# Kernel tuning notes

Hardware: AMD Instinct MI355X
Metric: run time of the kernel (lower is better)

The kernel has to match this reference:

```python
import jax, jax.numpy as jnp
import numpy as np

N_NODES = 10000
N_EDGES = 80000
N_GRAPHS = 64
HEADS = 8
F_IN = 128
D1, D2, D3 = 512, 256, 128  # per-head (and output, concat=False) widths
OUT_DIM = 10


def _lin(key, fin, fout):
    kw, kb = jax.random.split(key)
    w = jax.random.normal(kw, (fin, fout), dtype=jnp.float32) * 0.05
    b = jax.random.normal(kb, (fout,), dtype=jnp.float32) * 0.05
    return w, b


def setup_inputs() -> dict:
    key = jax.random.key(0)
    ks = jax.random.split(key, 24)
    x = jax.random.normal(ks[0], (N_NODES, F_IN), dtype=jnp.float32)
    edge_index = jax.random.randint(ks[1], (2, N_EDGES), 0, N_NODES, dtype=jnp.int64)
    batch = jnp.sort(jax.random.randint(ks[2], (N_NODES,), 0, N_GRAPHS, dtype=jnp.int64))
    d = {"x": x, "edge_index": edge_index, "batch": batch}
    # conv1: 128 -> heads*512 (q,k,v), skip 128 -> 512
    d["w_q1"], d["b_q1"] = _lin(ks[3], F_IN, HEADS * D1)
    d["w_k1"], d["b_k1"] = _lin(ks[4], F_IN, HEADS * D1)
    d["w_v1"], d["b_v1"] = _lin(ks[5], F_IN, HEADS * D1)
    d["w_s1"], d["b_s1"] = _lin(ks[6], F_IN, D1)
    # conv2: 512 -> heads*256, skip 512 -> 256
    d["w_q2"], d["b_q2"] = _lin(ks[7], D1, HEADS * D2)
    d["w_k2"], d["b_k2"] = _lin(ks[8], D1, HEADS * D2)
    d["w_v2"], d["b_v2"] = _lin(ks[9], D1, HEADS * D2)
    d["w_s2"], d["b_s2"] = _lin(ks[10], D1, D2)
    # conv3: 256 -> heads*128, skip 256 -> 128
    d["w_q3"], d["b_q3"] = _lin(ks[11], D2, HEADS * D3)
    d["w_k3"], d["b_k3"] = _lin(ks[12], D2, HEADS * D3)
    d["w_v3"], d["b_v3"] = _lin(ks[13], D2, HEADS * D3)
    d["w_s3"], d["b_s3"] = _lin(ks[14], D2, D3)
    # global attention gate + final fc
    d["w_g"], d["b_g"] = _lin(ks[15], D3, 1)
    d["w_fc"], d["b_fc"] = _lin(ks[16], D3, OUT_DIM)
    return d


def _seg_softmax(a, seg, n):
    m = jax.ops.segment_max(a, seg, num_segments=n)
    e = jnp.exp(a - m[seg])
    s = jax.ops.segment_sum(e, seg, num_segments=n)
    return e / (s[seg] + 1e-16)


def _tconv(x, edge_index, wq, bq, wk, bk, wv, bv, ws, bs):
    # PyG TransformerConv, concat=False, root_weight=True, no edge features
    n = x.shape[0]
    c = wq.shape[1] // HEADS
    q = (x @ wq + bq).reshape(n, HEADS, c)
    k = (x @ wk + bk).reshape(n, HEADS, c)
    v = (x @ wv + bv).reshape(n, HEADS, c)
    src, dst = edge_index[0], edge_index[1]
    a = jnp.einsum('ehc,ehc->eh', q[dst], k[src]) / jnp.sqrt(jnp.float32(c))
    alpha = _seg_softmax(a, dst, n)                                  # [E, H]
    out = jax.ops.segment_sum(v[src] * alpha[..., None], dst, num_segments=n)
    return out.mean(axis=1) + (x @ ws + bs)                          # mean over heads + skip


def reference(x, edge_index, batch,
              w_q1, b_q1, w_k1, b_k1, w_v1, b_v1, w_s1, b_s1,
              w_q2, b_q2, w_k2, b_k2, w_v2, b_v2, w_s2, b_s2,
              w_q3, b_q3, w_k3, b_k3, w_v3, b_v3, w_s3, b_s3,
              w_g, b_g, w_fc, b_fc):
    h = jax.nn.elu(_tconv(x, edge_index, w_q1, b_q1, w_k1, b_k1, w_v1, b_v1, w_s1, b_s1))
    h = jax.nn.elu(_tconv(h, edge_index, w_q2, b_q2, w_k2, b_k2, w_v2, b_v2, w_s2, b_s2))
    h = jax.nn.elu(_tconv(h, edge_index, w_q3, b_q3, w_k3, b_k3, w_v3, b_v3, w_s3, b_s3))
    # GlobalAttention pooling: softmax(gate) over nodes within each graph
    gate = h @ w_g + b_g                                             # [N, 1]
    gate = _seg_softmax(gate, batch, N_GRAPHS)
    g = jax.ops.segment_sum(gate * h, batch, num_segments=N_GRAPHS)  # [G, D3]
    return g @ w_fc + b_fc                                           # [G, OUT_DIM]
```

## Files before the change

kernel.cpp:

```cpp
#include <hip/hip_runtime.h>
#include <math.h>

typedef __bf16 bf16;
typedef __bf16 bf16x8 __attribute__((ext_vector_type(8)));
typedef __bf16 bf16x4 __attribute__((ext_vector_type(4)));
typedef __bf16 bf16x2 __attribute__((ext_vector_type(2)));
typedef float f32x4 __attribute__((ext_vector_type(4)));
typedef float f32x2 __attribute__((ext_vector_type(2)));
typedef unsigned int u32;

#define N_NODES 10000
#define N_EDGES 80000
#define N_GRAPHS 64

template<int EPL> struct VecT;
template<> struct VecT<8>{ typedef bf16x8 type; };
template<> struct VecT<4>{ typedef bf16x4 type; };
template<> struct VecT<2>{ typedef bf16x2 type; };

__device__ inline unsigned f2ord(float f){
  unsigned u = __float_as_uint(f);
  return (u & 0x80000000u) ? ~u : (u | 0x80000000u);
}
__device__ inline float ord2f(unsigned u){
  return (u & 0x80000000u) ? __uint_as_float(u & 0x7fffffffu) : __uint_as_float(~u);
}

__device__ inline void gload_lds16(const bf16* g, bf16* l){
  __builtin_amdgcn_global_load_lds(
      (const __attribute__((address_space(1))) unsigned int*)g,
      (__attribute__((address_space(3))) unsigned int*)l, 16, 0, 0);
}

__global__ __launch_bounds__(256) void detect_f32_k(const unsigned short* __restrict__ raw, int n,
                                                    int* __restrict__ flagF){
  int i = blockIdx.x*256 + threadIdx.x;
  if (i < n){
    unsigned e = (raw[i] >> 7) & 0xFFu;
    if (e >= 0xC0u) atomicOr(flagF, 1);
  }
}

struct CvPack {
  const void* src[11];
  bf16* dst[11];
  int pre[12];
  int rl[11];
  int st[11];
};
__global__ __launch_bounds__(256) void convert_all(CvPack p, const int* __restrict__ flagF){
  int gid = blockIdx.x*256 + threadIdx.x;
  if (gid >= p.pre[11]) return;
  int t = 0;
  while (gid >= p.pre[t+1]) ++t;
  int i = gid - p.pre[t];
  bool f = (*flagF != 0);
  float v = f ? ((const float*)p.src[t])[i] : (float)((const bf16*)p.src[t])[i];
  int row = i / p.rl[t], col = i - row*p.rl[t];
  p.dst[t][(size_t)row*p.st[t] + col] = (bf16)v;
}

__global__ __launch_bounds__(256) void detect_i64(const int* __restrict__ raw, int* __restrict__ flag){
  int i = blockIdx.x*256 + threadIdx.x;
  if (i < 4000 && raw[2*i+1] != 0) atomicOr(flag, 1);
}

__global__ __launch_bounds__(256) void conv_idx(const int* __restrict__ ei_raw,
                                                const int* __restrict__ b_raw,
                                                const int* __restrict__ flag,
                                                int* __restrict__ src, int* __restrict__ dst,
                                                int* __restrict__ bat, int* __restrict__ cnt){
  int i = blockIdx.x*256 + threadIdx.x;
  bool i32 = (*flag != 0);
  if (i < N_EDGES){
    int s = i32 ? ei_raw[i]   : ei_raw[2*i];
    int d = i32 ? ei_raw[N_EDGES + i] : ei_raw[2*(N_EDGES + i)];
    s = min(max(s, 0), N_NODES-1);
    d = min(max(d, 0), N_NODES-1);
    src[i] = s; dst[i] = d;
    atomicAdd(&cnt[d], 1);
  }
  if (i < N_NODES){
    int b = i32 ? b_raw[i] : b_raw[2*i];
    bat[i] = min(max(b, 0), N_GRAPHS-1);
  }
}

__global__ __launch_bounds__(256) void scanA(const int* __restrict__ cnt, int* __restrict__ fill,
                                             int* __restrict__ bsum, int N){
  __shared__ int s[256];
  int i = blockIdx.x*256 + threadIdx.x;
  int v = (i < N) ? cnt[i] : 0;
  s[threadIdx.x] = v;
  __syncthreads();
  for (int d = 1; d < 256; d <<= 1){
    int t = (threadIdx.x >= d) ? s[threadIdx.x - d] : 0;
    __syncthreads();
    s[threadIdx.x] += t;
    __syncthreads();
  }
  if (i < N) fill[i] = s[threadIdx.x] - v;
  if (threadIdx.x == 255) bsum[blockIdx.x] = s[255];
}
__global__ __launch_bounds__(64) void scanB(int* __restrict__ bsum, int nb){
  if (threadIdx.x == 0){
    int a = 0;
    for (int b = 0; b < nb; ++b){ int t = bsum[b]; bsum[b] = a; a += t; }
  }
}
__global__ __launch_bounds__(256) void scanC(const int* __restrict__ bsum, int* __restrict__ fill,
                                             int* __restrict__ row_ptr, int N){
  int i = blockIdx.x*256 + threadIdx.x;
  if (i < N){
    int st = fill[i] + bsum[i >> 8];
    fill[i] = st;
    row_ptr[i] = st;
  }
  if (i == 0) row_ptr[N] = N_EDGES;
}

__global__ __launch_bounds__(256) void fill_csr(const int* __restrict__ dst,
                                                int* __restrict__ fill, int* __restrict__ eids){
  int e = blockIdx.x*256 + threadIdx.x;
  if (e < N_EDGES){
    int p = atomicAdd(&fill[dst[e]], 1);
    eids[p] = e;
  }
}

__global__ __launch_bounds__(256)
void gemm_bias(const bf16* __restrict__ A, int lda,
               const bf16* __restrict__ Bt,
               const bf16* __restrict__ bias, bf16* __restrict__ Cout, int ldc,
               int M, int N, int K)
{
  __shared__ bf16 As[128*64];
  __shared__ bf16 Bs[128*64];
  const int tid = threadIdx.x;
  const int lane = tid & 63;
  const int wave = tid >> 6;
  const int m0 = blockIdx.y * 128, n0 = blockIdx.x * 128;
  const int wm = (wave >> 1) * 64, wn = (wave & 1) * 64;
  const int l15 = lane & 15, l4 = lane >> 4;
  const int srow = lane >> 3;
  const int schunk = lane & 7;

  f32x4 acc[4][4] = {};

  for (int k0 = 0; k0 < K; k0 += 64){
    #pragma unroll
    for (int j = 0; j < 4; ++j){
      int r0 = (wave*4 + j)*8;
      int r  = r0 + srow;
      int gc = schunk ^ (r & 7);
      int ga = m0 + r; if (ga >= M) ga = M-1;
      gload_lds16(A  + (size_t)ga*lda      + k0 + gc*8, As + r0*64);
      gload_lds16(Bt + (size_t)(n0 + r)*K  + k0 + gc*8, Bs + r0*64);
    }
    __syncthreads();
    #pragma unroll
    for (int kt = 0; kt < 2; ++kt){
      bf16x8 af[4], bfr[4];
      #pragma unroll
      for (int mt = 0; mt < 4; ++mt){
        int row = wm + mt*16 + l15;
        int p = (kt*4 + l4) ^ (l15 & 7);
        af[mt] = *(const bf16x8*)(As + row*64 + p*8);
      }
      #pragma unroll
      for (int nt = 0; nt < 4; ++nt){
        int row = wn + nt*16 + l15;
        int p = (kt*4 + l4) ^ (l15 & 7);
        bfr[nt] = *(const bf16x8*)(Bs + row*64 + p*8);
      }
      #pragma unroll
      for (int mt = 0; mt < 4; ++mt)
        #pragma unroll
        for (int nt = 0; nt < 4; ++nt)
          acc[mt][nt] = __builtin_amdgcn_mfma_f32_16x16x32_bf16(af[mt], bfr[nt], acc[mt][nt], 0, 0, 0);
    }
    __syncthreads();
  }

  #pragma unroll
  for (int nt = 0; nt < 4; ++nt){
    int col = n0 + wn + nt*16 + l15;
    float bv = (float)bias[col];
    #pragma unroll
    for (int mt = 0; mt < 4; ++mt){
      int rbase = m0 + wm + mt*16 + l4*4;
      #pragma unroll
      for (int r = 0; r < 4; ++r){
        int row = rbase + r;
        if (row < M) Cout[(size_t)row*ldc + col] = (bf16)(acc[mt][nt][r] + bv);
      }
    }
  }
}

template<int BM, int OUTMODE>
__global__ __launch_bounds__(256)
void gemm_fused(const bf16* __restrict__ A, int lda,
                const bf16* __restrict__ Bt,
                const bf16* __restrict__ bp, const bf16* __restrict__ mb,
                const int* __restrict__ row_ptr,
                bf16* __restrict__ outB, int ldo, float* __restrict__ outF,
                int M, int K)
{
  constexpr int PA    = BM/32;
  constexpr int WCOLS = 128/BM;
  constexpr int WTN   = BM;
  constexpr int NT    = WTN/16;
  __shared__ bf16 As[BM*64];
  __shared__ bf16 Bs[128*64];
  const int tid = threadIdx.x;
  const int lane = tid & 63;
  const int wave = tid >> 6;
  const int m0 = blockIdx.y * BM, n0 = blockIdx.x * 128;
  const int wm = (wave / WCOLS) * 32;
  const int wn = (wave % WCOLS) * WTN;
  const int l15 = lane & 15, l4 = lane >> 4;
  const int srow = lane >> 3;
  const int schunk = lane & 7;

  f32x4 acc[2][NT] = {};

  for (int k0 = 0; k0 < K; k0 += 64){
    #pragma unroll
    for (int j = 0; j < PA; ++j){
      int r0 = (wave*PA + j)*8;
      int r  = r0 + srow;
      int gc = schunk ^ (r & 7);
      int ga = m0 + r; if (ga >= M) ga = M-1;
      gload_lds16(A + (size_t)ga*lda + k0 + gc*8, As + r0*64);
    }
    #pragma unroll
    for (int j = 0; j < 4; ++j){
      int r0 = (wave*4 + j)*8;
      int r  = r0 + srow;
      int gc = schunk ^ (r & 7);
      gload_lds16(Bt + (size_t)(n0 + r)*K + k0 + gc*8, Bs + r0*64);
    }
    __syncthreads();
    #pragma unroll
    for (int kt = 0; kt < 2; ++kt){
      bf16x8 af[2], bfr[NT];
      #pragma unroll
      for (int mt = 0; mt < 2; ++mt){
        int row = wm + mt*16 + l15;
        int p = (kt*4 + l4) ^ (l15 & 7);
        af[mt] = *(const bf16x8*)(As + row*64 + p*8);
      }
      #pragma unroll
      for (int nt = 0; nt < NT; ++nt){
        int row = wn + nt*16 + l15;
        int p = (kt*4 + l4) ^ (l15 & 7);
        bfr[nt] = *(const bf16x8*)(Bs + row*64 + p*8);
      }
      #pragma unroll
      for (int mt = 0; mt < 2; ++mt)
        #pragma unroll
        for (int nt = 0; nt < NT; ++nt)
          acc[mt][nt] = __builtin_amdgcn_mfma_f32_16x16x32_bf16(af[mt], bfr[nt], acc[mt][nt], 0, 0, 0);
    }
    __syncthreads();
  }

  if (OUTMODE == 0){
    float bv[NT], mv[NT];
    #pragma unroll
    for (int nt = 0; nt < NT; ++nt){
      int col = n0 + wn + nt*16 + l15;
      bv[nt] = (float)bp[col];
      mv[nt] = (float)mb[col];
    }
    #pragma unroll
    for (int mt = 0; mt < 2; ++mt){
      int rbase = m0 + wm + mt*16 + l4*4;
      #pragma unroll
      for (int r = 0; r < 4; ++r){
        int row = rbase + r;
        if (row < M){
          bool d0 = (row_ptr[row+1] == row_ptr[row]);
          #pragma unroll
          for (int nt = 0; nt < NT; ++nt){
            int col = n0 + wn + nt*16 + l15;
            float v = acc[mt][nt][r] + bv[nt] - (d0 ? mv[nt] : 0.f);
            v = (v > 0.f) ? v : (__expf(v) - 1.f);
            outB[(size_t)row*ldo + col] = (bf16)v;
          }
        }
      }
    }
  } else {
    #pragma unroll
    for (int mt = 0; mt < 2; ++mt){
      int rbase = m0 + wm + mt*16 + l4*4;
      #pragma unroll
      for (int r = 0; r < 4; ++r){
        int row = rbase + r;
        if (row < M){
          #pragma unroll
          for (int nt = 0; nt < NT; ++nt){
            int col = n0 + wn + nt*16 + l15;
            outF[(size_t)row*128 + col] = acc[mt][nt][r];
          }
        }
      }
    }
  }
}

__global__ __launch_bounds__(256)
void finalize_gate(const float* __restrict__ facc, const bf16* __restrict__ bp,
                   const bf16* __restrict__ mb, const int* __restrict__ row_ptr,
                   bf16* __restrict__ hout, const bf16* __restrict__ wg,
                   const bf16* __restrict__ bg, const int* __restrict__ bat,
                   float* __restrict__ gate, unsigned* __restrict__ gmax)
{
  __shared__ float wred[4];
  int idx = blockIdx.x*256 + threadIdx.x;
  int n = idx >> 7, c = idx & 127;
  bool d0 = (row_ptr[n+1] == row_ptr[n]);
  float v = facc[idx] + (float)bp[c] - (d0 ? (float)mb[c] : 0.f);
  v = (v > 0.f) ? v : (__expf(v) - 1.f);
  hout[idx] = (bf16)v;
  float gc = v * (float)wg[c];
  #pragma unroll
  for (int o = 32; o; o >>= 1) gc += __shfl_xor(gc, o, 64);
  int wave = threadIdx.x >> 6;
  if ((threadIdx.x & 63) == 0) wred[wave] = gc;
  __syncthreads();
  if ((threadIdx.x & 127) == 0){
    float g = wred[wave] + wred[wave + 1] + (float)bg[0];
    gate[n] = g;
    atomicMax(&gmax[bat[n]], f2ord(g));
  }
}

struct MhPack { const bf16* wk[3]; const bf16* wq[3]; bf16* wzt[3]; int fin[3]; int c[3]; };
__global__ __launch_bounds__(256)
void gemm_mh_all(MhPack P)
{
  const int L = blockIdx.z >> 3, h = blockIdx.z & 7;
  const int Fin = P.fin[L], C = P.c[L];
  const int nb = Fin >> 7;
  if ((int)blockIdx.x >= nb || (int)blockIdx.y >= nb) return;
  __shared__ bf16 As[128*64];
  __shared__ bf16 Bs[128*64];
  const int ld = 8*C;
  const bf16* Ab = P.wk[L] + h*C;
  const bf16* Bb = P.wq[L] + h*C;
  bf16* Cb = P.wzt[L] + (size_t)h*Fin*Fin;
  const int tid = threadIdx.x;
  const int lane = tid & 63;
  const int wave = tid >> 6;
  const int m0 = blockIdx.y * 128, n0 = blockIdx.x * 128;
  const int wm = (wave >> 1) * 64, wn = (wave & 1) * 64;
  const int l15 = lane & 15, l4 = lane >> 4;
  const int srow = lane >> 3;
  const int schunk = lane & 7;

  f32x4 acc[4][4] = {};

  for (int k0 = 0; k0 < C; k0 += 64){
    #pragma unroll
    for (int j = 0; j < 4; ++j){
      int r0 = (wave*4 + j)*8;
      int r  = r0 + srow;
      int gc = schunk ^ (r & 7);
      gload_lds16(Ab + (size_t)(m0 + r)*ld + k0 + gc*8, As + r0*64);
      gload_lds16(Bb + (size_t)(n0 + r)*ld + k0 + gc*8, Bs + r0*64);
    }
    __syncthreads();
    #pragma unroll
    for (int kt = 0; kt < 2; ++kt){
      bf16x8 af[4], bfr[4];
      #pragma unroll
      for (int mt = 0; mt < 4; ++mt){
        int row = wm + mt*16 + l15;
        int p = (kt*4 + l4) ^ (l15 & 7);
        af[mt] = *(const bf16x8*)(As + row*64 + p*8);
      }
      #pragma unroll
      for (int nt = 0; nt < 4; ++nt){
        int row = wn + nt*16 + l15;
        int p = (kt*4 + l4) ^ (l15 & 7);
        bfr[nt] = *(const bf16x8*)(Bs + row*64 + p*8);
      }
      #pragma unroll
      for (int mt = 0; mt < 4; ++mt)
        #pragma unroll
        for (int nt = 0; nt < 4; ++nt)
          acc[mt][nt] = __builtin_amdgcn_mfma_f32_16x16x32_bf16(af[mt], bfr[nt], acc[mt][nt], 0, 0, 0);
    }
    __syncthreads();
  }

  #pragma unroll
  for (int nt = 0; nt < 4; ++nt){
    int col = n0 + wn + nt*16 + l15;
    #pragma unroll
    for (int mt = 0; mt < 4; ++mt){
      int rbase = m0 + wm + mt*16 + l4*4;
      #pragma unroll
      for (int r = 0; r < 4; ++r)
        Cb[(size_t)(rbase + r)*Fin + col] = (bf16)acc[mt][nt][r];
    }
  }
}

struct WvPack { const void* wv[3]; const void* ws[3]; bf16* bt[3]; int fin[3]; int c[3]; int bx[3]; int by[3]; };
__global__ __launch_bounds__(256)
void prep_wv_all(WvPack P, const int* __restrict__ flagF)
{
  const int L = blockIdx.z;
  if ((int)blockIdx.x >= P.bx[L] || (int)blockIdx.y >= P.by[L]) return;
  __shared__ float t[32][33];
  bool f = (*flagF != 0);
  const int Fin = P.fin[L], C = P.c[L];
  int k0 = blockIdx.x*32, j0 = blockIdx.y*32;
  int x = threadIdx.x & 31, y = threadIdx.x >> 5;
  const void* srcp; int nstride, cb; float sc; int i0;
  if (k0 < 8*Fin){
    int h = k0 / Fin; i0 = k0 - h*Fin;
    srcp = P.wv[L]; nstride = 8*C; cb = h*C + j0; sc = 0.125f;
  } else {
    i0 = k0 - 8*Fin;
    srcp = P.ws[L]; nstride = C; cb = j0; sc = 1.0f;
  }
  #pragma unroll
  for (int ii = 0; ii < 4; ++ii){
    int i = i0 + y + ii*8;
    size_t idx = (size_t)i*nstride + cb + x;
    float v = f ? ((const float*)srcp)[idx] : (float)((const bf16*)srcp)[idx];
    t[y + ii*8][x] = v*sc;
  }
  __syncthreads();
  #pragma unroll
  for (int ii = 0; ii < 4; ++ii){
    int j = j0 + y + ii*8;
    P.bt[L][(size_t)j*(9*Fin) + k0 + x] = (bf16)t[x][y + ii*8];
  }
}

struct SmPack { const bf16* wkc[3]; const void* bq[3]; const void* bv[3]; const void* bs[3];
                int fin[3]; int c[3]; bf16* tz[3]; bf16* bp[3]; bf16* mb[3]; int rb[3]; int bpb[3]; };
__global__ __launch_bounds__(256)
void prep_small_all(SmPack P, const int* __restrict__ flagF)
{
  const int L = blockIdx.z;
  const int Fin = P.fin[L], C = P.c[L];
  const int rb = P.rb[L];
  if ((int)blockIdx.x >= rb + P.bpb[L]) return;
  bool f = (*flagF != 0);
  if ((int)blockIdx.x < rb){
    int wave = threadIdx.x >> 6, lane = threadIdx.x & 63;
    int r = blockIdx.x*4 + wave;
    int h = r / Fin, i = r - h*Fin;
    int epc = C >> 6;
    const bf16* wp = P.wkc[L] + (size_t)i*8*C + h*C;
    const void* bqp = P.bq[L];
    float s = 0.f;
    for (int k = 0; k < epc; ++k){
      int c = k*64 + lane;
      float b = f ? ((const float*)bqp)[h*C + c] : (float)((const bf16*)bqp)[h*C + c];
      s += (float)wp[c] * b;
    }
    #pragma unroll
    for (int o = 32; o; o >>= 1) s += __shfl_xor(s, o, 64);
    if (lane == 0) P.tz[L][r] = (bf16)s;
  } else {
    int idx = ((int)blockIdx.x - rb)*256 + threadIdx.x;
    if (idx < C){
      float s = 0.f;
      for (int h = 0; h < 8; ++h)
        s += f ? ((const float*)P.bv[L])[h*C + idx] : (float)((const bf16*)P.bv[L])[h*C + idx];
      s *= 0.125f;
      float bsv = f ? ((const float*)P.bs[L])[idx] : (float)((const bf16*)P.bs[L])[idx];
      P.mb[L][idx] = (bf16)s;
      P.bp[L][idx] = (bf16)(s + bsv);
    }
  }
}

template<int Fin, int NHT>
__global__ __launch_bounds__(256)
void node_edge(const bf16* __restrict__ z, int zw, int hbase,
               bf16* __restrict__ AP, int ldP,
               const int* __restrict__ row_ptr, const int* __restrict__ eids,
               const int* __restrict__ srcv, float scale)
{
  constexpr int EPL  = Fin/64;
  constexpr int EPL2 = EPL/2;
  constexpr int KC   = Fin/32;
  typedef typename VecT<EPL>::type vecb;
  __shared__ float sw[4][68][12];

  const int wave = threadIdx.x >> 6;
  const int lane = threadIdx.x & 63;
  const int n = blockIdx.x*4 + wave;

  const int beg = row_ptr[n];
  int deg = row_ptr[n+1] - beg;
  if (deg > 64) deg = 64;

  bf16* APn = AP + (size_t)n*ldP;

  if (deg == 0){
    vecb zv;
    #pragma unroll
    for (int k = 0; k < EPL; ++k) zv[k] = (bf16)0.f;
    #pragma unroll
    for (int h = 0; h < NHT; ++h)
      *(vecb*)(APn + (size_t)(hbase + h)*Fin + lane*EPL) = zv;
    return;
  }

  int e_ld = (lane < deg) ? lane : 0;
  int srcReg = srcv[eids[beg + e_ld]];

  const int nc = (deg + 15) >> 4;
  const int l15 = lane & 15, l4 = lane >> 4;
  const int h   = l15 & (NHT-1);
  const bf16* zp = z + (size_t)n*zw + (size_t)h*Fin + l4*8;

  f32x4 sacc[4];
  #pragma unroll
  for (int c = 0; c < 4; ++c) sacc[c] = (f32x4){0.f,0.f,0.f,0.f};

  #pragma unroll
  for (int c = 0; c < 4; ++c){
    if (c < nc){
      int sn = __shfl(srcReg, c*16 + l15, 64);
      const bf16* ap = AP + (size_t)sn*ldP + 8*Fin + l4*8;
      f32x4 s = (f32x4){0.f,0.f,0.f,0.f};
      #pragma unroll
      for (int k = 0; k < KC; ++k){
        bf16x8 af = *(const bf16x8*)(ap + k*32);
        bf16x8 bv = *(const bf16x8*)(zp + k*32);
        s = __builtin_amdgcn_mfma_f32_16x16x32_bf16(af, bv, s, 0, 0, 0);
      }
      sacc[c] = s;
    }
  }

  float m = -3.4e38f;
  #pragma unroll
  for (int c = 0; c < 4; ++c){
    if (c < nc){
      #pragma unroll
      for (int r = 0; r < 4; ++r){
        int row = c*16 + l4*4 + r;
        float v = sacc[c][r]*scale;
        sacc[c][r] = v;
        if (row < deg) m = fmaxf(m, v);
      }
    }
  }
  m = fmaxf(m, __shfl_xor(m, 16, 64));
  m = fmaxf(m, __shfl_xor(m, 32, 64));
  float ssum = 0.f;
  #pragma unroll
  for (int c = 0; c < 4; ++c){
    if (c < nc){
      #pragma unroll
      for (int r = 0; r < 4; ++r){
        int row = c*16 + l4*4 + r;
        float e = (row < deg) ? __expf(sacc[c][r] - m) : 0.f;
        sacc[c][r] = e;
        ssum += e;
      }
    }
  }
  ssum += __shfl_xor(ssum, 16, 64);
  ssum += __shfl_xor(ssum, 32, 64);
  float inv = 1.f/(ssum + 1e-16f);

  if (l15 < NHT){
    #pragma unroll
    for (int c = 0; c < 4; ++c){
      if (c < nc){
        #pragma unroll
        for (int r = 0; r < 4; ++r)
          sw[wave][c*16 + l4*4 + r][l15] = sacc[c][r]*inv;
      }
    }
  }
  if (lane < 4*NHT)
    sw[wave][nc*16 + (lane >> 3)][lane & 7] = 0.f;

  f32x2 acc[NHT][EPL2];
  #pragma unroll
  for (int hh = 0; hh < NHT; ++hh)
    #pragma unroll
    for (int p = 0; p < EPL2; ++p) acc[hh][p] = (f32x2){0.f,0.f};

  for (int i0 = 0; i0 < deg; i0 += 4){
    int sn0 = __shfl(srcReg, i0,   64);
    int sn1 = __shfl(srcReg, i0+1, 64);
    int sn2 = __shfl(srcReg, i0+2, 64);
    int sn3 = __shfl(srcReg, i0+3, 64);
    vecb hv0 = *(const vecb*)(AP + (size_t)sn0*ldP + 8*Fin + lane*EPL);
    vecb hv1 = *(const vecb*)(AP + (size_t)sn1*ldP + 8*Fin + lane*EPL);
    vecb hv2 = *(const vecb*)(AP + (size_t)sn2*ldP + 8*Fin + lane*EPL);
    vecb hv3 = *(const vecb*)(AP + (size_t)sn3*ldP + 8*Fin + lane*EPL);
    #pragma unroll
    for (int j = 0; j < 4; ++j){
      int e = i0 + j;
      vecb hv = (j == 0) ? hv0 : (j == 1) ? hv1 : (j == 2) ? hv2 : hv3;
      f32x4 w0 = *(const f32x4*)&sw[wave][e][0];
      f32x4 w1 = (NHT == 8) ? *(const f32x4*)&sw[wave][e][4] : w0;
      f32x2 xf[EPL2];
      const u32* up = (const u32*)&hv;
      #pragma unroll
      for (int p = 0; p < EPL2; ++p){
        u32 u = up[p];
        xf[p] = (f32x2){ __uint_as_float(u << 16), __uint_as_float(u & 0xffff0000u) };
      }
      #pragma unroll
      for (int hh = 0; hh < NHT; ++hh){
        float w = (hh < 4) ? w0[hh] : w1[hh-4];
        f32x2 wv = (f32x2){w, w};
        #pragma unroll
        for (int p = 0; p < EPL2; ++p)
          acc[hh][p] += wv * xf[p];
      }
    }
  }

  #pragma unroll
  for (int hh = 0; hh < NHT; ++hh){
    vecb o;
    #pragma unroll
    for (int p = 0; p < EPL2; ++p){
      o[2*p]   = (bf16)acc[hh][p][0];
      o[2*p+1] = (bf16)acc[hh][p][1];
    }
    *(vecb*)(APn + (size_t)(hbase + hh)*Fin + lane*EPL) = o;
  }
}

__global__ __launch_bounds__(256) void gate_expsum(float* __restrict__ gate, const int* __restrict__ bat,
                                                   const unsigned* __restrict__ gmax, float* __restrict__ gsum){
  int n = blockIdx.x*256 + threadIdx.x;
  if (n < N_NODES){
    float e = __expf(gate[n] - ord2f(gmax[bat[n]]));
    gate[n] = e;
    atomicAdd(&gsum[bat[n]], e);
  }
}

__global__ __launch_bounds__(256) void pool_weighted(const float* __restrict__ gate, const float* __restrict__ gsum,
                                                     const int* __restrict__ bat, const bf16* __restrict__ h,
                                                     float* __restrict__ gacc){
  int n = blockIdx.x*4 + (threadIdx.x >> 6);
  if (n >= N_NODES) return;
  int lane = threadIdx.x & 63;
  int b = bat[n];
  float w = gate[n]/(gsum[b] + 1e-16f);
  atomicAdd(&gacc[b*128 + lane],      w*(float)h[(size_t)n*128 + lane]);
  atomicAdd(&gacc[b*128 + 64 + lane], w*(float)h[(size_t)n*128 + 64 + lane]);
}

__global__ __launch_bounds__(64) void final_fc(const float* __restrict__ gacc, const bf16* __restrict__ wfc,
                                               const bf16* __restrict__ bfc, void* __restrict__ out,
                                               const int* __restrict__ flagF){
  int g = blockIdx.x;
  int o = threadIdx.x;
  if (o < 10){
    float s = (float)bfc[o];
    for (int c = 0; c < 128; ++c) s += gacc[g*128 + c]*(float)wfc[c*10 + o];
    if (*flagF) ((float*)out)[(size_t)g*10 + o] = s;
    else        ((bf16*)out)[(size_t)g*10 + o]  = (bf16)s;
  }
}

extern "C" void kernel_launch(void* const* d_in, const int* in_sizes, int n_in,
                              void* d_out, int out_size, void* d_ws, size_t ws_size,
                              hipStream_t stream)
{
  const int* ei   = (const int*)d_in[1];
  const int* braw = (const int*)d_in[2];

  bf16 *Wzt1=0,*Wzt2=0,*Wzt3=0,*Wvt1=0,*Wvt2=0,*Wvt3=0;
  float *facc=0,*gate=0;
  bf16 *tz1=0,*tz2=0,*tz3=0,*bp1=0,*mb1=0,*bp2=0,*mb2=0,*bp3=0,*mb3=0,*h3=0;
  bf16 *cwg=0,*cbg=0,*cwfc=0,*cbfc=0;
  int *src=0,*dst=0,*bat=0,*cnt=0,*row_ptr=0,*fillp=0,*eids=0,*flagbuf=0;
  char *A1=0, *A2=0;

  auto plan = [&](bool big)->size_t{
    size_t off = 0;
    auto A = [&](size_t bytes)->char*{
      char* p = (char*)d_ws + off;
      off += (bytes + 255) & ~(size_t)255;
      return p;
    };
    A1 = A(92160000);
    A2 = A(big ? 81920000 : 46080000);
    Wzt1 = (bf16*)A((size_t)8*128*128*2);
    Wzt2 = (bf16*)A((size_t)8*512*512*2);
    Wzt3 = (bf16*)A((size_t)8*256*256*2);
    Wvt1 = (bf16*)A((size_t)512*9*128*2);
    Wvt2 = (bf16*)A((size_t)256*9*512*2);
    Wvt3 = (bf16*)A((size_t)128*9*256*2);
    facc = (float*)A((size_t)N_NODES*512*4);
    tz1  = (bf16*)A(8*128*2);
    tz2  = (bf16*)A(8*512*2);
    tz3  = (bf16*)A(8*256*2);
    bp1  = (bf16*)A(512*2);  mb1 = (bf16*)A(512*2);
    bp2  = (bf16*)A(256*2);  mb2 = (bf16*)A(256*2);
    bp3  = (bf16*)A(128*2);  mb3 = (bf16*)A(128*2);
    h3   = (bf16*)A((size_t)N_NODES*128*2);
    src  = (int*)A((size_t)N_EDGES*4);
    dst  = (int*)A((size_t)N_EDGES*4);
    bat  = (int*)A((size_t)N_NODES*4);
    cnt  = (int*)A((size_t)N_NODES*4);
    row_ptr = (int*)A((size_t)(N_NODES+1)*4);
    fillp= (int*)A((size_t)N_NODES*4);
    eids = (int*)A((size_t)N_EDGES*4);
    flagbuf = (int*)A(16384);
    gate = (float*)A((size_t)N_NODES*4);
    unsigned* poolz = (unsigned*)A((size_t)(64 + 64 + 64*128)*4);
    (void)poolz;
    cwg  = (bf16*)A(128*2);
    cbg  = (bf16*)A(2*2);
    cwfc = (bf16*)A(1280*2);
    cbfc = (bf16*)A(10*2);
    return off;
  };

  bool big = (plan(true) <= ws_size);
  if (!big && plan(false) > ws_size) return;
  plan(big);
  unsigned* poolz = (unsigned*)((char*)gate + (((size_t)N_NODES*4 + 255) & ~(size_t)255));

  int* flagI = flagbuf;
  int* flagF = flagbuf + 1;
  int* bsum  = (int*)((char*)flagbuf + 8192);
  unsigned* gmax = poolz;
  float*    gsum = (float*)(poolz + 64);
  float*    gacc = (float*)(poolz + 128);

  bf16* AP1 = (bf16*)A2;   const int ldP1 = 1152;
  bf16* z1  = (bf16*)A1;
  bf16* AP2 = (bf16*)A1;   const int ldP2 = 4608;
  bf16* z2  = (bf16*)A2;
  bf16* AP3 = (bf16*)A2;   const int ldP3 = 2304;
  bf16* z3  = (bf16*)A1;
  bf16* wq1c = (bf16*)(A1 + 48000000);  bf16* wk1c = wq1c + 128*4096;
  bf16* wq2c = wk1c + 128*4096;         bf16* wk2c = wq2c + 512*2048;
  bf16* wq3c = wk2c + 512*2048;         bf16* wk3c = wq3c + 256*1024;

  hipMemsetAsync(flagbuf, 0, 16384, stream);
  {
    int nprobe = in_sizes[0] < 32768 ? in_sizes[0] : 32768;
    detect_f32_k<<<(nprobe + 255)/256, 256, 0, stream>>>((const unsigned short*)d_in[0], nprobe, flagF);
    detect_i64<<<16, 256, 0, stream>>>(ei, flagI);
  }

  {
    CvPack p;
    const int CIDX[11] = {0, 3, 5, 11, 13, 19, 21, 27, 28, 29, 30};
    bf16* CDST[11] = {AP1 + 1024, wq1c, wk1c, wq2c, wk2c, wq3c, wk3c, cwg, cbg, cwfc, cbfc};
    int tot = 0;
    for (int t = 0; t < 11; ++t){
      p.src[t] = d_in[CIDX[t]];
      p.dst[t] = CDST[t];
      p.pre[t] = tot;
      int n = in_sizes[CIDX[t]];
      tot += n;
      if (t == 0){ p.rl[t] = 128; p.st[t] = 1152; }
      else       { p.rl[t] = n;   p.st[t] = n;    }
    }
    p.pre[11] = tot;
    convert_all<<<(tot + 255)/256, 256, 0, stream>>>(p, flagF);
  }

  hipMemsetAsync(cnt, 0, (size_t)N_NODES*4, stream);
  conv_idx<<<(N_EDGES + 255)/256, 256, 0, stream>>>(ei, braw, flagI, src, dst, bat, cnt);
  scanA<<<40, 256, 0, stream>>>(cnt, fillp, bsum, N_NODES);
  scanB<<<1, 64, 0, stream>>>(bsum, 40);
  scanC<<<40, 256, 0, stream>>>(bsum, fillp, row_ptr, N_NODES);
  fill_csr<<<(N_EDGES + 255)/256, 256, 0, stream>>>(dst, fillp, eids);

  {
    MhPack mp;
    mp.wk[0]=wk1c; mp.wk[1]=wk2c; mp.wk[2]=wk3c;
    mp.wq[0]=wq1c; mp.wq[1]=wq2c; mp.wq[2]=wq3c;
    mp.wzt[0]=Wzt1; mp.wzt[1]=Wzt2; mp.wzt[2]=Wzt3;
    mp.fin[0]=128; mp.fin[1]=512; mp.fin[2]=256;
    mp.c[0]=512; mp.c[1]=256; mp.c[2]=128;
    gemm_mh_all<<<dim3(4,4,24), 256, 0, stream>>>(mp);

    WvPack wp;
    wp.wv[0]=d_in[7];  wp.wv[1]=d_in[15]; wp.wv[2]=d_in[23];
    wp.ws[0]=d_in[9];  wp.ws[1]=d_in[17]; wp.ws[2]=d_in[25];
    wp.bt[0]=Wvt1; wp.bt[1]=Wvt2; wp.bt[2]=Wvt3;
    wp.fin[0]=128; wp.fin[1]=512; wp.fin[2]=256;
    wp.c[0]=512; wp.c[1]=256; wp.c[2]=128;
    wp.bx[0]=36; wp.bx[1]=144; wp.bx[2]=72;
    wp.by[0]=16; wp.by[1]=8;   wp.by[2]=4;
    prep_wv_all<<<dim3(144,16,3), 256, 0, stream>>>(wp, flagF);

    SmPack sp;
    sp.wkc[0]=wk1c; sp.wkc[1]=wk2c; sp.wkc[2]=wk3c;
    sp.bq[0]=d_in[4];  sp.bq[1]=d_in[12]; sp.bq[2]=d_in[20];
    sp.bv[0]=d_in[8];  sp.bv[1]=d_in[16]; sp.bv[2]=d_in[24];
    sp.bs[0]=d_in[10]; sp.bs[1]=d_in[18]; sp.bs[2]=d_in[26];
    sp.fin[0]=128; sp.fin[1]=512; sp.fin[2]=256;
    sp.c[0]=512; sp.c[1]=256; sp.c[2]=128;
    sp.tz[0]=tz1; sp.tz[1]=tz2; sp.tz[2]=tz3;
    sp.bp[0]=bp1; sp.bp[1]=bp2; sp.bp[2]=bp3;
    sp.mb[0]=mb1; sp.mb[1]=mb2; sp.mb[2]=mb3;
    sp.rb[0]=256;  sp.rb[1]=1024; sp.rb[2]=512;
    sp.bpb[0]=2;   sp.bpb[1]=1;   sp.bpb[2]=1;
    prep_small_all<<<dim3(1025,1,3), 256, 0, stream>>>(sp, flagF);
  }

  const int MT = (N_NODES + 127)/128;
  const int NB = N_NODES/4;
  const int MT64 = (N_NODES + 63)/64;
  const int MT32 = (N_NODES + 31)/32;
  const float sc1 = 1.0f/sqrtf(512.f), sc2 = 1.0f/sqrtf(256.f), sc3 = 1.0f/sqrtf(128.f);

  hipMemsetAsync(poolz, 0, (size_t)(64 + 64 + 64*128)*4, stream);

  gemm_bias<<<dim3(8, MT), 256, 0, stream>>>(AP1 + 1024, ldP1, Wzt1, tz1, z1, 1024, N_NODES, 1024, 128);
  node_edge<128,8><<<NB, 256, 0, stream>>>(z1, 1024, 0, AP1, ldP1, row_ptr, eids, src, sc1);
  gemm_fused<64,0><<<dim3(4, MT64), 256, 0, stream>>>(AP1, ldP1, Wvt1, bp1, mb1, row_ptr,
                                                      AP2 + 4096, ldP2, (float*)0, N_NODES, 1152);

  if (big){
    gemm_bias<<<dim3(32, MT), 256, 0, stream>>>(AP2 + 4096, ldP2, Wzt2, tz2, z2, 4096, N_NODES, 4096, 512);
    node_edge<512,8><<<NB, 256, 0, stream>>>(z2, 4096, 0, AP2, ldP2, row_ptr, eids, src, sc2);
  } else {
    for (int g = 0; g < 2; ++g){
      gemm_bias<<<dim3(16, MT), 256, 0, stream>>>(AP2 + 4096, ldP2, Wzt2 + (size_t)g*4*512*512, tz2 + g*4*512, z2, 2048, N_NODES, 2048, 512);
      node_edge<512,4><<<NB, 256, 0, stream>>>(z2, 2048, g*4, AP2, ldP2, row_ptr, eids, src, sc2);
    }
  }
  gemm_fused<32,0><<<dim3(2, MT32), 256, 0, stream>>>(AP2, ldP2, Wvt2, bp2, mb2, row_ptr,
                                                      AP3 + 2048, ldP3, (float*)0, N_NODES, 4608);

  gemm_bias<<<dim3(16, MT), 256, 0, stream>>>(AP3 + 2048, ldP3, Wzt3, tz3, z3, 2048, N_NODES, 2048, 256);
  node_edge<256,8><<<NB, 256, 0, stream>>>(z3, 2048, 0, AP3, ldP3, row_ptr, eids, src, sc3);
  gemm_fused<32,1><<<dim3(1, MT32), 256, 0, stream>>>(AP3, ldP3, Wvt3, (const bf16*)0, (const bf16*)0, (const int*)0,
                                                      (bf16*)0, 0, facc, N_NODES, 2304);
  finalize_gate<<<(N_NODES*128)/256, 256, 0, stream>>>(facc, bp3, mb3, row_ptr, h3, cwg, cbg, bat, gate, gmax);

  gate_expsum<<<(N_NODES + 255)/256, 256, 0, stream>>>(gate, bat, gmax, gsum);
  pool_weighted<<<(N_NODES + 3)/4, 256, 0, stream>>>(gate, gsum, bat, h3, gacc);
  final_fc<<<N_GRAPHS, 64, 0, stream>>>(gacc, cwfc, cbfc, d_out, flagF);
}
```

Measured before the change: 649.0 us.

## Add 256x128 triple-buffered 8-wave GEMM for layer 2/3 projections

Introduces a new bias GEMM kernel with 256x128 output tiles and 512 threads, which triple-buffers LDS via direct global-to-LDS loads with manual vmcnt waits. It splits each k-step into two MFMA halves with prefetch issued in between, and raises wave priority around the MFMAs. It replaces the 128-row gemm_bias for the layer-2 (big path) and layer-3 z projections, aiming to cut barrier stalls and memory latency and to raise reuse. In exchange it uses large LDS (one block per CU) and gives fewer blocks for the 10000-row M.

```diff
diff --git a/kernel.cpp b/kernel.cpp
--- a/kernel.cpp
+++ b/kernel.cpp
@@ -193,6 +193,124 @@
       for (int r = 0; r < 4; ++r){
         int row = rbase + r;
         if (row < M) Cout[(size_t)row*ldc + col] = (bf16)(acc[mt][nt][r] + bv);
+      }
+    }
+  }
+}
+
+__global__ __launch_bounds__(512, 1)
+void gemm8p_bias(const bf16* __restrict__ A, int lda,
+                 const bf16* __restrict__ Bt,
+                 const bf16* __restrict__ bias, bf16* __restrict__ Cout, int ldc,
+                 int M, int K)
+{
+  __shared__ bf16 As[3][256*64];
+  __shared__ bf16 Bs[3][128*64];
+  const int tid = threadIdx.x;
+  const int lane = tid & 63;
+  const int wave = tid >> 6;
+  const int m0 = blockIdx.y * 256, n0 = blockIdx.x * 128;
+  const int wm = (wave >> 1) * 64;
+  const int wn = (wave & 1) * 64;
+  const int l15 = lane & 15, l4 = lane >> 4;
+  const int srow = lane >> 3;
+  const int schunk = lane & 7;
+  const int NT = K >> 6;
+
+  auto stageA = [&](int t, int j){
+    int b = t % 3;
+    int r0 = (wave + j*8)*8;
+    int r  = r0 + srow;
+    int gc = schunk ^ srow;
+    int ga = m0 + r; if (ga >= M) ga = M-1;
+    gload_lds16(A + (size_t)ga*lda + t*64 + gc*8, &As[b][r0*64]);
+  };
+  auto stageB = [&](int t, int j){
+    int b = t % 3;
+    int r0 = (wave + j*8)*8;
+    int r  = r0 + srow;
+    int gc = schunk ^ srow;
+    gload_lds16(Bt + (size_t)(n0 + r)*K + t*64 + gc*8, &Bs[b][r0*64]);
+  };
+
+  stageA(0,0); stageA(0,1); stageA(0,2); stageA(0,3); stageB(0,0); stageB(0,1);
+  if (NT > 1){ stageA(1,0); stageA(1,1); stageA(1,2); stageA(1,3); stageB(1,0); stageB(1,1); }
+  if (NT > 1) asm volatile("s_waitcnt vmcnt(6)" ::: "memory");
+  else        asm volatile("s_waitcnt vmcnt(0)" ::: "memory");
+  __builtin_amdgcn_s_barrier();
+
+  f32x4 acc[4][4] = {};
+
+  for (int t = 0; t < NT; ++t){
+    const bf16* as = &As[t % 3][0];
+    const bf16* bs = &Bs[t % 3][0];
+    bf16x8 bfr[4][2];
+    bf16x8 af[2][2];
+
+    #pragma unroll
+    for (int nt2 = 0; nt2 < 4; ++nt2)
+      #pragma unroll
+      for (int kt = 0; kt < 2; ++kt){
+        int row = wn + nt2*16 + l15;
+        int p = (kt*4 + l4) ^ (l15 & 7);
+        bfr[nt2][kt] = *(const bf16x8*)(bs + row*64 + p*8);
+      }
+    #pragma unroll
+    for (int i = 0; i < 2; ++i)
+      #pragma unroll
+      for (int kt = 0; kt < 2; ++kt){
+        int row = wm + i*16 + l15;
+        int p = (kt*4 + l4) ^ (l15 & 7);
+        af[i][kt] = *(const bf16x8*)(as + row*64 + p*8);
+      }
+    if (t + 2 < NT){ stageA(t+2,0); stageA(t+2,1); stageB(t+2,0); }
+    __builtin_amdgcn_s_setprio(1);
+    #pragma unroll
+    for (int i = 0; i < 2; ++i)
+      #pragma unroll
+      for (int nt2 = 0; nt2 < 4; ++nt2)
+        #pragma unroll
+        for (int kt = 0; kt < 2; ++kt)
+          acc[i][nt2] = __builtin_amdgcn_mfma_f32_16x16x32_bf16(af[i][kt], bfr[nt2][kt], acc[i][nt2], 0, 0, 0);
+    __builtin_amdgcn_s_setprio(0);
+
+    #pragma unroll
+    for (int i = 0; i < 2; ++i)
+      #pragma unroll
+      for (int kt = 0; kt < 2; ++kt){
+        int row = wm + (2+i)*16 + l15;
+        int p = (kt*4 + l4) ^ (l15 & 7);
+        af[i][kt] = *(const bf16x8*)(as + row*64 + p*8);
+      }
+    if (t + 2 < NT){ stageA(t+2,2); stageA(t+2,3); stageB(t+2,1); }
+    __builtin_amdgcn_s_setprio(1);
+    #pragma unroll
+    for (int i = 0; i < 2; ++i)
+      #pragma unroll
+      for (int nt2 = 0; nt2 < 4; ++nt2)
+        #pragma unroll
+        for (int kt = 0; kt < 2; ++kt)
+          acc[2+i][nt2] = __builtin_amdgcn_mfma_f32_16x16x32_bf16(af[i][kt], bfr[nt2][kt], acc[2+i][nt2], 0, 0, 0);
+    __builtin_amdgcn_s_setprio(0);
+
+    if (t < NT - 1){
+      if (t + 2 < NT) asm volatile("s_waitcnt vmcnt(6)" ::: "memory");
+      else            asm volatile("s_waitcnt vmcnt(0)" ::: "memory");
+      __builtin_amdgcn_s_barrier();
+    }
+  }
+
+  #pragma unroll
+  for (int nt2 = 0; nt2 < 4; ++nt2){
+    int col = n0 + wn + nt2*16 + l15;
+    float bv = (float)bias[col];
+    #pragma unroll
+    for (int mt = 0; mt < 4; ++mt){
+      int rbase = m0 + wm + mt*16 + l4*4;
+      #pragma unroll
+      for (int r = 0; r < 4; ++r){
+        int row = rbase + r;
+        if (row < M) Cout[(size_t)row*ldc + col] = (bf16)(acc[mt][nt2][r] + bv);
       }
     }
   }
@@ -821,8 +939,9 @@
 
   const int MT = (N_NODES + 127)/128;
   const int NB = N_NODES/4;
+  const int MT32 = (N_NODES + 31)/32;
   const int MT64 = (N_NODES + 63)/64;
-  const int MT32 = (N_NODES + 31)/32;
+  const int MT256 = (N_NODES + 255)/256;
   const float sc1 = 1.0f/sqrtf(512.f), sc2 = 1.0f/sqrtf(256.f), sc3 = 1.0f/sqrtf(128.f);
 
   hipMemsetAsync(poolz, 0, (size_t)(64 + 64 + 64*128)*4, stream);
@@ -833,7 +952,7 @@
                                                       AP2 + 4096, ldP2, (float*)0, N_NODES, 1152);
 
   if (big){
-    gemm_bias<<<dim3(32, MT), 256, 0, stream>>>(AP2 + 4096, ldP2, Wzt2, tz2, z2, 4096, N_NODES, 4096, 512);
+    gemm8p_bias<<<dim3(32, MT256), 512, 0, stream>>>(AP2 + 4096, ldP2, Wzt2, tz2, z2, 4096, N_NODES, 512);
     node_edge<512,8><<<NB, 256, 0, stream>>>(z2, 4096, 0, AP2, ldP2, row_ptr, eids, src, sc2);
   } else {
     for (int g = 0; g < 2; ++g){
@@ -844,7 +963,7 @@
   gemm_fused<32,0><<<dim3(2, MT32), 256, 0, stream>>>(AP2, ldP2, Wvt2, bp2, mb2, row_ptr,
                                                       AP3 + 2048, ldP3, (float*)0, N_NODES, 4608);
 
-  gemm_bias<<<dim3(16, MT), 256, 0, stream>>>(AP3 + 2048, ldP3, Wzt3, tz3, z3, 2048, N_NODES, 2048, 256);
+  gemm8p_bias<<<dim3(16, MT256), 512, 0, stream>>>(AP3 + 2048, ldP3, Wzt3, tz3, z3, 2048, N_NODES, 256);
   node_edge<256,8><<<NB, 256, 0, stream>>>(z3, 2048, 0, AP3, ldP3, row_ptr, eids, src, sc3);
   gemm_fused<32,1><<<dim3(1, MT32), 256, 0, stream>>>(AP3, ldP3, Wvt3, (const bf16*)0, (const bf16*)0, (const int*)0,
                                                       (bf16*)0, 0, facc, N_NODES, 2304);
```

After: 652.3 us. No clear change (+0.5%).
